# Performance work log

Measured on AMD Instinct MI355X. Metric: run time of the kernel, lower is better.

Reference implementation:

```python
import jax, jax.numpy as jnp
import numpy as np

D_MODEL = 1024
N_HEADS = 16
D_K = D_MODEL // N_HEADS


def setup_inputs() -> dict:
    key = jax.random.key(0)
    ks = jax.random.split(key, 12)
    B, S = 2, 2048
    scale = 1.0 / np.sqrt(D_MODEL)
    inp = {
        "q": jax.random.normal(ks[0], (B, S, D_MODEL), jnp.float32),
        "k": jax.random.normal(ks[1], (B, S, D_MODEL), jnp.float32),
        "v": jax.random.normal(ks[2], (B, S, D_MODEL), jnp.float32),
        "k_pe": jax.random.normal(ks[3], (N_HEADS, D_K, S), jnp.float32),
        "Wq": jax.random.normal(ks[4], (D_MODEL, D_MODEL), jnp.float32) * scale,
        "bq": jnp.zeros((D_MODEL,), jnp.float32),
        "Wk": jax.random.normal(ks[5], (D_MODEL, D_MODEL), jnp.float32) * scale,
        "bk": jnp.zeros((D_MODEL,), jnp.float32),
        "Wv": jax.random.normal(ks[6], (D_MODEL, D_MODEL), jnp.float32) * scale,
        "bv": jnp.zeros((D_MODEL,), jnp.float32),
        "Wo": jax.random.normal(ks[7], (D_MODEL, D_MODEL), jnp.float32) * scale,
        "bo": jnp.zeros((D_MODEL,), jnp.float32),
    }
    return inp


def reference(q, k, v, k_pe, Wq, bq, Wk, bk, Wv, bv, Wo, bo):
    B, S, _ = q.shape
    # projections -> [B, H, S, d_k]
    def split_heads(x):
        return x.reshape(B, S, N_HEADS, D_K).transpose(0, 2, 1, 3)
    qh = split_heads(q @ Wq + bq)
    kh = split_heads(k @ Wk + bk)
    vh = split_heads(v @ Wv + bv)
    # content scores + relative positional scores (two matmuls, summed)
    scores = jnp.einsum("bhsd,bhtd->bhst", qh, kh)
    scores = scores + jnp.einsum("bhsd,hdt->bhst", qh, k_pe)
    scores = scores / jnp.sqrt(jnp.asarray(D_K, qh.dtype))
    attn = jax.nn.softmax(scores, axis=-1)
    out = jnp.einsum("bhst,bhtd->bhsd", attn, vh)  # [B,H,S,d_k]
    out = out.transpose(0, 2, 1, 3).reshape(B, S, D_MODEL)
    return out @ Wo + bo
```

## Files before the change

### kernel.cpp

```cpp
#include <hip/hip_runtime.h>
#include <stdint.h>
#include <math.h>

typedef __bf16 bf16;
typedef __attribute__((ext_vector_type(8))) __bf16 bf16x8;
typedef __attribute__((ext_vector_type(4))) __bf16 bf16x4;
typedef __attribute__((ext_vector_type(4))) float f32x4;

#define MFMA_BF16(a, b, c) __builtin_amdgcn_mfma_f32_16x16x32_bf16((a), (b), (c), 0, 0, 0)

#if __has_builtin(__builtin_amdgcn_exp2f)
#define EXP2F __builtin_amdgcn_exp2f
#else
#define EXP2F exp2f
#endif

#define QSCALE 0.18033688011112042f

__device__ __forceinline__ void gl_lds16(const bf16* g, bf16* l) {
  __builtin_amdgcn_global_load_lds(
      (__attribute__((address_space(1))) unsigned int*)(uintptr_t)(g),
      (__attribute__((address_space(3))) unsigned int*)(l),
      16, 0, 0);
}

__global__ __launch_bounds__(256) void prep(
    const float* __restrict__ q, const float* __restrict__ k,
    const float* __restrict__ v, bf16* __restrict__ qb,
    bf16* __restrict__ kb, bf16* __restrict__ vb,
    const float* __restrict__ W0, const float* __restrict__ W1,
    const float* __restrict__ W2, const float* __restrict__ W3,
    bf16* __restrict__ Wt,
    const float* __restrict__ kpe, bf16* __restrict__ kpeb)
{
  __shared__ float tile[64][65];
  const int tid = threadIdx.x;
  const int bid = blockIdx.x;
  if (bid < 6144) {
    const int z = bid >> 11;
    const int idx = bid & 2047;
    const float* s = (z == 0) ? q : (z == 1) ? k : v;
    bf16* d = (z == 0) ? qb : (z == 1) ? kb : vb;
    size_t i = ((size_t)idx * 256 + tid) * 8;
    float4 a = *(const float4*)(s + i);
    float4 b = *(const float4*)(s + i + 4);
    bf16x8 o;
    o[0] = (bf16)a.x; o[1] = (bf16)a.y; o[2] = (bf16)a.z; o[3] = (bf16)a.w;
    o[4] = (bf16)b.x; o[5] = (bf16)b.y; o[6] = (bf16)b.z; o[7] = (bf16)b.w;
    *(bf16x8*)(d + i) = o;
  } else if (bid < 7168) {
    const int t = bid - 6144;
    const int z = t >> 8;
    const int rem = t & 255;
    const int r0 = (rem >> 4) * 64, c0 = (rem & 15) * 64;
    const float* src = (z == 0) ? W0 : (z == 1) ? W1 : (z == 2) ? W2 : W3;
    bf16* dst = Wt + (size_t)z * (1024 * 1024);
#pragma unroll
    for (int h = 0; h < 2; ++h) {
      int qq = tid + h * 256;
      int row = qq >> 3, cc = qq & 7;
      float4 a = *(const float4*)(src + (size_t)(r0 + row) * 1024 + c0 + cc * 8);
      float4 b = *(const float4*)(src + (size_t)(r0 + row) * 1024 + c0 + cc * 8 + 4);
      tile[row][cc * 8 + 0] = a.x; tile[row][cc * 8 + 1] = a.y;
      tile[row][cc * 8 + 2] = a.z; tile[row][cc * 8 + 3] = a.w;
      tile[row][cc * 8 + 4] = b.x; tile[row][cc * 8 + 5] = b.y;
      tile[row][cc * 8 + 6] = b.z; tile[row][cc * 8 + 7] = b.w;
    }
    __syncthreads();
#pragma unroll
    for (int h = 0; h < 2; ++h) {
      int qq = tid + h * 256;
      int row = qq >> 3, cc = qq & 7;
      bf16x8 o;
#pragma unroll
      for (int e = 0; e < 8; ++e) o[e] = (bf16)tile[cc * 8 + e][row];
      *(bf16x8*)(dst + (size_t)(c0 + row) * 1024 + r0 + cc * 8) = o;
    }
  } else {
    const int idx = bid - 7168;
    size_t i = ((size_t)idx * 256 + tid) * 8;
    float4 a = *(const float4*)(kpe + i);
    float4 b = *(const float4*)(kpe + i + 4);
    bf16x8 o;
    o[0] = (bf16)a.x; o[1] = (bf16)a.y; o[2] = (bf16)a.z; o[3] = (bf16)a.w;
    o[4] = (bf16)b.x; o[5] = (bf16)b.y; o[6] = (bf16)b.z; o[7] = (bf16)b.w;
    *(bf16x8*)(kpeb + i) = o;
  }
}

template <int MODE>
__device__ __forceinline__ void gemm_body(
    const bf16* __restrict__ A, const bf16* __restrict__ Wt,
    const float* __restrict__ bias, float oscale,
    const bf16* __restrict__ kpeb, void* __restrict__ out_v,
    bf16* __restrict__ As, bf16* __restrict__ Bs)
{
  const int tid = threadIdx.x;
  const int w = tid >> 6, lane = tid & 63;
  const int lm = lane & 15, quad = lane >> 4;
  const int wr = w >> 1, wc = w & 1;
  const int lid = blockIdx.x + (blockIdx.y << 3);
  const int xcd = lid & 7, j = lid >> 3;
  const int m0 = (xcd * 4 + (j & 3)) * 128;
  const int n0 = (j >> 2) * 128;

  f32x4 zero4 = {0.f, 0.f, 0.f, 0.f};
  f32x4 acc[4][4];
#pragma unroll
  for (int i = 0; i < 4; ++i)
#pragma unroll
    for (int jj = 0; jj < 4; ++jj) acc[i][jj] = zero4;

  auto stage = [&](int buf, int kb) {
#pragma unroll
    for (int h = 0; h < 2; ++h) {
      int qq = tid + h * 256;
      int row = qq >> 2, cs = qq & 3;
      int cc = cs ^ ((row >> 1) & 3);
      gl_lds16(A + (size_t)(m0 + row) * 1024 + kb * 32 + cc * 8,
               As + buf * 4096 + qq * 8);
      gl_lds16(Wt + (size_t)(n0 + row) * 1024 + kb * 32 + cc * 8,
               Bs + buf * 4096 + qq * 8);
    }
  };

  stage(0, 0);
  stage(1, 1);

  int cur = 0;
  for (int kb = 0; kb < 32; ++kb) {
    if (kb < 30) {
      stage((kb + 2) % 3, kb + 2);
      asm volatile("s_waitcnt vmcnt(8)" ::: "memory");
    } else if (kb == 30) {
      asm volatile("s_waitcnt vmcnt(4)" ::: "memory");
    } else {
      asm volatile("s_waitcnt vmcnt(0)" ::: "memory");
    }
    __builtin_amdgcn_s_barrier();
    asm volatile("" ::: "memory");

    const bf16* Ab = As + cur * 4096;
    const bf16* Bb = Bs + cur * 4096;
    bf16x8 af[4], bfv[4];
#pragma unroll
    for (int i = 0; i < 4; ++i) {
      int row = wr * 64 + i * 16 + lm;
      af[i] = *(const bf16x8*)(Ab + row * 32 + ((quad ^ ((row >> 1) & 3)) * 8));
    }
#pragma unroll
    for (int jj = 0; jj < 4; ++jj) {
      int row = wc * 64 + jj * 16 + lm;
      bfv[jj] = *(const bf16x8*)(Bb + row * 32 + ((quad ^ ((row >> 1) & 3)) * 8));
    }
#pragma unroll
    for (int i = 0; i < 4; ++i)
#pragma unroll
      for (int jj = 0; jj < 4; ++jj)
        acc[i][jj] = MFMA_BF16(af[i], bfv[jj], acc[i][jj]);

    __builtin_amdgcn_s_barrier();
    asm volatile("" ::: "memory");
    cur = (cur + 1) == 3 ? 0 : cur + 1;
  }

  const int ncol = n0 + wc * 64;
  float bv4[4];
#pragma unroll
  for (int jj = 0; jj < 4; ++jj) bv4[jj] = bias[ncol + jj * 16 + lm];
#pragma unroll
  for (int i = 0; i < 4; ++i) {
    const int mbase = m0 + wr * 64 + i * 16 + quad * 4;
    const int b = mbase >> 11, s = mbase & 2047;
#pragma unroll
    for (int jj = 0; jj < 4; ++jj) {
      const int ng = ncol + jj * 16 + lm;
      const int hh = ng >> 6, d = ng & 63;
      if (MODE == 2) {
        bf16x4 o;
#pragma unroll
        for (int r = 0; r < 4; ++r) o[r] = (bf16)(acc[i][jj][r] + bv4[jj]);
        *(bf16x4*)((bf16*)out_v + ((size_t)(b * 16 + hh) * 64 + d) * 2048 + s) = o;
      } else if (MODE == 1) {
        bf16x4 p4 = *(const bf16x4*)(kpeb + ((size_t)(hh * 64 + d)) * 2048 + s);
#pragma unroll
        for (int r = 0; r < 4; ++r) {
          float val = acc[i][jj][r] + bv4[jj] + (float)p4[r];
          ((bf16*)out_v)[(((size_t)(b * 16 + hh)) * 2048 + (s + r)) * 64 + d] =
              (bf16)val;
        }
      } else if (MODE == 0) {
#pragma unroll
        for (int r = 0; r < 4; ++r) {
          float val = acc[i][jj][r] + bv4[jj];
          ((bf16*)out_v)[(((size_t)(b * 16 + hh)) * 2048 + (s + r)) * 64 + d] =
              (bf16)(val * oscale);
        }
      } else {
#pragma unroll
        for (int r = 0; r < 4; ++r) {
          float val = acc[i][jj][r] + bv4[jj];
          ((float*)out_v)[(size_t)(mbase + r) * 1024 + ng] = val;
        }
      }
    }
  }
}

__global__ __launch_bounds__(256) void qkv_gemm(
    const bf16* __restrict__ qb, const bf16* __restrict__ kb, const bf16* __restrict__ vb,
    const bf16* __restrict__ Wt, const float* __restrict__ biq,
    const float* __restrict__ bik, const float* __restrict__ biv,
    const bf16* __restrict__ kpeb,
    bf16* __restrict__ Qs, bf16* __restrict__ Ks, bf16* __restrict__ Vts)
{
  __shared__ __align__(16) bf16 As[3 * 128 * 32];
  __shared__ __align__(16) bf16 Bs[3 * 128 * 32];
  const int z = blockIdx.z;
  if (z == 0) {
    gemm_body<0>(qb, Wt, biq, QSCALE, nullptr, Qs, As, Bs);
  } else if (z == 1) {
    gemm_body<1>(kb, Wt + (size_t)1 * 1024 * 1024, bik, 1.f, kpeb, Ks, As, Bs);
  } else {
    gemm_body<2>(vb, Wt + (size_t)2 * 1024 * 1024, biv, 1.f, nullptr, Vts, As, Bs);
  }
}

__global__ __launch_bounds__(256) void out_gemm(
    const bf16* __restrict__ A, const bf16* __restrict__ Wt,
    const float* __restrict__ bias, float* __restrict__ out)
{
  __shared__ __align__(16) bf16 As[3 * 128 * 32];
  __shared__ __align__(16) bf16 Bs[3 * 128 * 32];
  gemm_body<3>(A, Wt, bias, 1.f, nullptr, out, As, Bs);
}

__global__ __launch_bounds__(512) void flash_attn(
    const bf16* __restrict__ Q, const bf16* __restrict__ K,
    const bf16* __restrict__ Vt, bf16* __restrict__ O)
{
  __shared__ __align__(16) bf16 QtPs[128 * 72];
  __shared__ __align__(16) bf16 Kt[2][64 * 64];
  __shared__ __align__(16) bf16 Vs[2][64 * 64];
  bf16* Ps = QtPs;

  const int tid = threadIdx.x;
  const int w = tid >> 6, lane = tid & 63;
  const int lm = lane & 15, quad = lane >> 4;
  const int id = blockIdx.x;
  const int xcd = id & 7, j = id >> 3;
  const int bh = xcd * 4 + (j & 3);
  const int s0 = (j >> 2) * 128;
  const size_t qkbase = (size_t)bh * (2048 * 64);
  const size_t vbase = (size_t)bh * (64 * 2048);

#pragma unroll
  for (int h = 0; h < 2; ++h) {
    int qq = tid + h * 512;
    int row = qq >> 3, cs = qq & 7;
    int cc = cs ^ (row & 7);
    gl_lds16(Q + qkbase + (size_t)(s0 + row) * 64 + cc * 8, QtPs + qq * 8);
  }
  {
    int row = tid >> 3, cs = tid & 7;
    int cc = cs ^ (row & 7);
    gl_lds16(K + qkbase + (size_t)row * 64 + cc * 8, Kt[0] + tid * 8);
    gl_lds16(Vt + vbase + (size_t)row * 2048 + cc * 8, Vs[0] + tid * 8);
  }
  __syncthreads();

  bf16x8 qa0, qa1;
  {
    int row = w * 16 + lm;
    qa0 = *(const bf16x8*)(QtPs + row * 64 + ((quad ^ (row & 7)) * 8));
    qa1 = *(const bf16x8*)(QtPs + row * 64 + (((quad + 4) ^ (row & 7)) * 8));
  }
  __syncthreads();

  f32x4 zero4 = {0.f, 0.f, 0.f, 0.f};
  float l_part = 0.f;
  f32x4 oacc[4];
#pragma unroll
  for (int dt = 0; dt < 4; ++dt) oacc[dt] = zero4;

  const int prow = (w * 16 + lm) * 72;

  for (int kt = 0; kt < 32; ++kt) {
    const int cur = kt & 1;
    if (kt < 31) {
      const int t1 = (kt + 1) * 64;
      int row = tid >> 3, cs = tid & 7;
      int cc = cs ^ (row & 7);
      gl_lds16(K + qkbase + (size_t)(t1 + row) * 64 + cc * 8, Kt[cur ^ 1] + tid * 8);
      gl_lds16(Vt + vbase + (size_t)row * 2048 + t1 + cc * 8, Vs[cur ^ 1] + tid * 8);
    }

#pragma unroll
    for (int c = 0; c < 4; ++c) {
      int row = c * 16 + lm;
      bf16x8 kb0 = *(const bf16x8*)(Kt[cur] + row * 64 + ((quad ^ (row & 7)) * 8));
      bf16x8 kb1 = *(const bf16x8*)(Kt[cur] + row * 64 + (((quad + 4) ^ (row & 7)) * 8));
      __builtin_amdgcn_s_setprio(1);
      f32x4 z = MFMA_BF16(kb0, qa0, zero4);
      f32x4 st = MFMA_BF16(kb1, qa1, z);
      __builtin_amdgcn_s_setprio(0);
      bf16x4 pk;
#pragma unroll
      for (int r = 0; r < 4; ++r) {
        float p = EXP2F(st[r]);
        l_part += p;
        pk[r] = (bf16)p;
      }
      *(bf16x4*)(Ps + prow + c * 16 + quad * 4) = pk;
    }

    bf16x8 pa0 = *(const bf16x8*)(Ps + prow + quad * 8);
    bf16x8 pa1 = *(const bf16x8*)(Ps + prow + 32 + quad * 8);
#pragma unroll
    for (int dt = 0; dt < 4; ++dt) {
      int row = dt * 16 + lm;
      bf16x8 va0 = *(const bf16x8*)(Vs[cur] + row * 64 + ((quad ^ (row & 7)) * 8));
      bf16x8 va1 = *(const bf16x8*)(Vs[cur] + row * 64 + (((quad + 4) ^ (row & 7)) * 8));
      __builtin_amdgcn_s_setprio(1);
      oacc[dt] = MFMA_BF16(va0, pa0, oacc[dt]);
      oacc[dt] = MFMA_BF16(va1, pa1, oacc[dt]);
      __builtin_amdgcn_s_setprio(0);
    }

    __syncthreads();
  }

  float l = l_part;
  l += __shfl_xor(l, 16, 64);
  l += __shfl_xor(l, 32, 64);
  float inv = 1.f / l;
#pragma unroll
  for (int dt = 0; dt < 4; ++dt)
#pragma unroll
    for (int r = 0; r < 4; ++r)
      Ps[prow + dt * 16 + quad * 4 + r] = (bf16)(oacc[dt][r] * inv);

  const int b = bh >> 4, hh = bh & 15;
  const int srow = s0 + w * 16 + lm;
  const size_t ob = ((size_t)(b * 2048 + srow)) * 1024 + hh * 64;
#pragma unroll
  for (int half = 0; half < 2; ++half) {
    bf16x8 ov = *(const bf16x8*)(Ps + prow + (half * 4 + quad) * 8);
    *(bf16x8*)(O + ob + (half * 4 + quad) * 8) = ov;
  }
}

extern "C" void kernel_launch(void* const* d_in, const int* in_sizes, int n_in,
                              void* d_out, int out_size, void* d_ws, size_t ws_size,
                              hipStream_t stream) {
  (void)in_sizes; (void)n_in; (void)out_size; (void)ws_size;
  const float* q   = (const float*)d_in[0];
  const float* k   = (const float*)d_in[1];
  const float* v   = (const float*)d_in[2];
  const float* kpe = (const float*)d_in[3];
  const float* Wq  = (const float*)d_in[4];
  const float* bq  = (const float*)d_in[5];
  const float* Wk  = (const float*)d_in[6];
  const float* bk  = (const float*)d_in[7];
  const float* Wv  = (const float*)d_in[8];
  const float* bv  = (const float*)d_in[9];
  const float* Wo  = (const float*)d_in[10];
  const float* bo  = (const float*)d_in[11];

  const size_t NT = 4u * 1024 * 1024;
  bf16* ws  = (bf16*)d_ws;
  bf16* Wt  = ws;
  bf16* qb  = Wt + NT;
  bf16* kb  = qb + NT;
  bf16* vb  = kb + NT;
  bf16* Qs  = vb + NT;
  bf16* Ks  = Qs + NT;
  bf16* Vts = Ks + NT;
  bf16* Oa  = Vts + NT;
  bf16* kpeb = Oa;

  prep<<<dim3(8192), 256, 0, stream>>>(q, k, v, qb, kb, vb, Wq, Wk, Wv, Wo, Wt,
                                       kpe, kpeb);
  qkv_gemm<<<dim3(8, 32, 3), 256, 0, stream>>>(qb, kb, vb, Wt, bq, bk, bv, kpeb,
                                               Qs, Ks, Vts);
  flash_attn<<<dim3(512), 512, 0, stream>>>(Qs, Ks, Vts, Oa);
  out_gemm<<<dim3(8, 32), 256, 0, stream>>>(Oa, Wt + 3u * 1024 * 1024, bo,
                                            (float*)d_out);
}
```

Measured before the change: 236.4 us.

## Enlarge QKV projection GEMM tiles to 256x256 with 512-thread blocks

```diff
diff --git a/kernel.cpp b/kernel.cpp
--- a/kernel.cpp
+++ b/kernel.cpp
@@ -89,7 +89,7 @@
 }
 
 template <int MODE>
-__device__ __forceinline__ void gemm_body(
+__device__ __forceinline__ void gemm_body256(
     const bf16* __restrict__ A, const bf16* __restrict__ Wt,
     const float* __restrict__ bias, float oscale,
     const bf16* __restrict__ kpeb, void* __restrict__ out_v,
@@ -99,28 +99,28 @@
   const int w = tid >> 6, lane = tid & 63;
   const int lm = lane & 15, quad = lane >> 4;
   const int wr = w >> 1, wc = w & 1;
-  const int lid = blockIdx.x + (blockIdx.y << 3);
-  const int xcd = lid & 7, j = lid >> 3;
-  const int m0 = (xcd * 4 + (j & 3)) * 128;
-  const int n0 = (j >> 2) * 128;
+  const int lid = blockIdx.x + (blockIdx.y << 2);
+  const int xcd = lid & 7, jj = lid >> 3;
+  const int m0 = (xcd * 2 + (jj & 1)) * 256;
+  const int n0 = (jj >> 1) * 256;
 
   f32x4 zero4 = {0.f, 0.f, 0.f, 0.f};
-  f32x4 acc[4][4];
+  f32x4 acc[4][8];
 #pragma unroll
   for (int i = 0; i < 4; ++i)
 #pragma unroll
-    for (int jj = 0; jj < 4; ++jj) acc[i][jj] = zero4;
+    for (int j = 0; j < 8; ++j) acc[i][j] = zero4;
 
   auto stage = [&](int buf, int kb) {
 #pragma unroll
     for (int h = 0; h < 2; ++h) {
-      int qq = tid + h * 256;
+      int qq = tid + h * 512;
       int row = qq >> 2, cs = qq & 3;
       int cc = cs ^ ((row >> 1) & 3);
       gl_lds16(A + (size_t)(m0 + row) * 1024 + kb * 32 + cc * 8,
-               As + buf * 4096 + qq * 8);
+               As + buf * 8192 + qq * 8);
       gl_lds16(Wt + (size_t)(n0 + row) * 1024 + kb * 32 + cc * 8,
-               Bs + buf * 4096 + qq * 8);
+               Bs + buf * 8192 + qq * 8);
     }
   };
 
@@ -140,89 +140,83 @@
     __builtin_amdgcn_s_barrier();
     asm volatile("" ::: "memory");
 
-    const bf16* Ab = As + cur * 4096;
-    const bf16* Bb = Bs + cur * 4096;
-    bf16x8 af[4], bfv[4];
+    const bf16* Ab = As + cur * 8192;
+    const bf16* Bb = Bs + cur * 8192;
+    bf16x8 af[4], bfv[8];
 #pragma unroll
     for (int i = 0; i < 4; ++i) {
       int row = wr * 64 + i * 16 + lm;
       af[i] = *(const bf16x8*)(Ab + row * 32 + ((quad ^ ((row >> 1) & 3)) * 8));
     }
 #pragma unroll
-    for (int jj = 0; jj < 4; ++jj) {
-      int row = wc * 64 + jj * 16 + lm;
-      bfv[jj] = *(const bf16x8*)(Bb + row * 32 + ((quad ^ ((row >> 1) & 3)) * 8));
+    for (int j = 0; j < 8; ++j) {
+      int row = wc * 128 + j * 16 + lm;
+      bfv[j] = *(const bf16x8*)(Bb + row * 32 + ((quad ^ ((row >> 1) & 3)) * 8));
     }
 #pragma unroll
     for (int i = 0; i < 4; ++i)
 #pragma unroll
-      for (int jj = 0; jj < 4; ++jj)
-        acc[i][jj] = MFMA_BF16(af[i], bfv[jj], acc[i][jj]);
+      for (int j = 0; j < 8; ++j)
+        acc[i][j] = MFMA_BF16(af[i], bfv[j], acc[i][j]);
 
     __builtin_amdgcn_s_barrier();
     asm volatile("" ::: "memory");
     cur = (cur + 1) == 3 ? 0 : cur + 1;
   }
 
-  const int ncol = n0 + wc * 64;
-  float bv4[4];
-#pragma unroll
-  for (int jj = 0; jj < 4; ++jj) bv4[jj] = bias[ncol + jj * 16 + lm];
+  const int ncol = n0 + wc * 128;
+  float bv8[8];
+#pragma unroll
+  for (int j = 0; j < 8; ++j) bv8[j] = bias[ncol + j * 16 + lm];
 #pragma unroll
   for (int i = 0; i < 4; ++i) {
     const int mbase = m0 + wr * 64 + i * 16 + quad * 4;
     const int b = mbase >> 11, s = mbase & 2047;
 #pragma unroll
-    for (int jj = 0; jj < 4; ++jj) {
-      const int ng = ncol + jj * 16 + lm;
+    for (int j = 0; j < 8; ++j) {
+      const int ng = ncol + j * 16 + lm;
       const int hh = ng >> 6, d = ng & 63;
       if (MODE == 2) {
         bf16x4 o;
 #pragma unroll
-        for (int r = 0; r < 4; ++r) o[r] = (bf16)(acc[i][jj][r] + bv4[jj]);
+        for (int r = 0; r < 4; ++r) o[r] = (bf16)(acc[i][j][r] + bv8[j]);
         *(bf16x4*)((bf16*)out_v + ((size_t)(b * 16 + hh) * 64 + d) * 2048 + s) = o;
       } else if (MODE == 1) {
         bf16x4 p4 = *(const bf16x4*)(kpeb + ((size_t)(hh * 64 + d)) * 2048 + s);
 #pragma unroll
         for (int r = 0; r < 4; ++r) {
-          float val = acc[i][jj][r] + bv4[jj] + (float)p4[r];
+          float val = acc[i][j][r] + bv8[j] + (float)p4[r];
           ((bf16*)out_v)[(((size_t)(b * 16 + hh)) * 2048 + (s + r)) * 64 + d] =
               (bf16)val;
         }
-      } else if (MODE == 0) {
+      } else {
 #pragma unroll
         for (int r = 0; r < 4; ++r) {
-          float val = acc[i][jj][r] + bv4[jj];
+          float val = acc[i][j][r] + bv8[j];
           ((bf16*)out_v)[(((size_t)(b * 16 + hh)) * 2048 + (s + r)) * 64 + d] =
               (bf16)(val * oscale);
         }
-      } else {
-#pragma unroll
-        for (int r = 0; r < 4; ++r) {
-          float val = acc[i][jj][r] + bv4[jj];
-          ((float*)out_v)[(size_t)(mbase + r) * 1024 + ng] = val;
-        }
       }
     }
   }
 }
 
-__global__ __launch_bounds__(256) void qkv_gemm(
+__global__ __launch_bounds__(512, 2) void qkv_gemm(
     const bf16* __restrict__ qb, const bf16* __restrict__ kb, const bf16* __restrict__ vb,
     const bf16* __restrict__ Wt, const float* __restrict__ biq,
     const float* __restrict__ bik, const float* __restrict__ biv,
     const bf16* __restrict__ kpeb,
     bf16* __restrict__ Qs, bf16* __restrict__ Ks, bf16* __restrict__ Vts)
 {
-  __shared__ __align__(16) bf16 As[3 * 128 * 32];
-  __shared__ __align__(16) bf16 Bs[3 * 128 * 32];
+  __shared__ __align__(16) bf16 As[3 * 256 * 32];
+  __shared__ __align__(16) bf16 Bs[3 * 256 * 32];
   const int z = blockIdx.z;
   if (z == 0) {
-    gemm_body<0>(qb, Wt, biq, QSCALE, nullptr, Qs, As, Bs);
+    gemm_body256<0>(qb, Wt, biq, QSCALE, nullptr, Qs, As, Bs);
   } else if (z == 1) {
-    gemm_body<1>(kb, Wt + (size_t)1 * 1024 * 1024, bik, 1.f, kpeb, Ks, As, Bs);
+    gemm_body256<1>(kb, Wt + (size_t)1 * 1024 * 1024, bik, 1.f, kpeb, Ks, As, Bs);
   } else {
-    gemm_body<2>(vb, Wt + (size_t)2 * 1024 * 1024, biv, 1.f, nullptr, Vts, As, Bs);
+    gemm_body256<2>(vb, Wt + (size_t)2 * 1024 * 1024, biv, 1.f, nullptr, Vts, As, Bs);
   }
 }
 
@@ -232,7 +226,91 @@
 {
   __shared__ __align__(16) bf16 As[3 * 128 * 32];
   __shared__ __align__(16) bf16 Bs[3 * 128 * 32];
-  gemm_body<3>(A, Wt, bias, 1.f, nullptr, out, As, Bs);
+  const int tid = threadIdx.x;
+  const int w = tid >> 6, lane = tid & 63;
+  const int lm = lane & 15, quad = lane >> 4;
+  const int wr = w >> 1, wc = w & 1;
+  const int lid = blockIdx.x + (blockIdx.y << 3);
+  const int xcd = lid & 7, j = lid >> 3;
+  const int m0 = (xcd * 4 + (j & 3)) * 128;
+  const int n0 = (j >> 2) * 128;
+
+  f32x4 zero4 = {0.f, 0.f, 0.f, 0.f};
+  f32x4 acc[4][4];
+#pragma unroll
+  for (int i = 0; i < 4; ++i)
+#pragma unroll
+    for (int jj = 0; jj < 4; ++jj) acc[i][jj] = zero4;
+
+  auto stage = [&](int buf, int kb) {
+#pragma unroll
+    for (int h = 0; h < 2; ++h) {
+      int qq = tid + h * 256;
+      int row = qq >> 2, cs = qq & 3;
+      int cc = cs ^ ((row >> 1) & 3);
+      gl_lds16(A + (size_t)(m0 + row) * 1024 + kb * 32 + cc * 8,
+               As + buf * 4096 + qq * 8);
+      gl_lds16(Wt + (size_t)(n0 + row) * 1024 + kb * 32 + cc * 8,
+               Bs + buf * 4096 + qq * 8);
+    }
+  };
+
+  stage(0, 0);
+  stage(1, 1);
+
+  int cur = 0;
+  for (int kb = 0; kb < 32; ++kb) {
+    if (kb < 30) {
+      stage((kb + 2) % 3, kb + 2);
+      asm volatile("s_waitcnt vmcnt(8)" ::: "memory");
+    } else if (kb == 30) {
+      asm volatile("s_waitcnt vmcnt(4)" ::: "memory");
+    } else {
+      asm volatile("s_waitcnt vmcnt(0)" ::: "memory");
+    }
+    __builtin_amdgcn_s_barrier();
+    asm volatile("" ::: "memory");
+
+    const bf16* Ab = As + cur * 4096;
+    const bf16* Bb = Bs + cur * 4096;
+    bf16x8 af[4], bfv[4];
+#pragma unroll
+    for (int i = 0; i < 4; ++i) {
+      int row = wr * 64 + i * 16 + lm;
+      af[i] = *(const bf16x8*)(Ab + row * 32 + ((quad ^ ((row >> 1) & 3)) * 8));
+    }
+#pragma unroll
+    for (int jj = 0; jj < 4; ++jj) {
+      int row = wc * 64 + jj * 16 + lm;
+      bfv[jj] = *(const bf16x8*)(Bb + row * 32 + ((quad ^ ((row >> 1) & 3)) * 8));
+    }
+#pragma unroll
+    for (int i = 0; i < 4; ++i)
+#pragma unroll
+      for (int jj = 0; jj < 4; ++jj)
+        acc[i][jj] = MFMA_BF16(af[i], bfv[jj], acc[i][jj]);
+
+    __builtin_amdgcn_s_barrier();
+    asm volatile("" ::: "memory");
+    cur = (cur + 1) == 3 ? 0 : cur + 1;
+  }
+
+  const int ncol = n0 + wc * 64;
+  float bv4[4];
+#pragma unroll
+  for (int jj = 0; jj < 4; ++jj) bv4[jj] = bias[ncol + jj * 16 + lm];
+#pragma unroll
+  for (int i = 0; i < 4; ++i) {
+    const int mbase = m0 + wr * 64 + i * 16 + quad * 4;
+#pragma unroll
+    for (int jj = 0; jj < 4; ++jj) {
+      const int ng = ncol + jj * 16 + lm;
+#pragma unroll
+      for (int r = 0; r < 4; ++r) {
+        out[(size_t)(mbase + r) * 1024 + ng] = acc[i][jj][r] + bv4[jj];
+      }
+    }
+  }
 }
 
 __global__ __launch_bounds__(512) void flash_attn(
@@ -381,7 +459,7 @@
 
   prep<<<dim3(8192), 256, 0, stream>>>(q, k, v, qb, kb, vb, Wq, Wk, Wv, Wo, Wt,
                                        kpe, kpeb);
-  qkv_gemm<<<dim3(8, 32, 3), 256, 0, stream>>>(qb, kb, vb, Wt, bq, bk, bv, kpeb,
+  qkv_gemm<<<dim3(4, 16, 3), 512, 0, stream>>>(qb, kb, vb, Wt, bq, bk, bv, kpeb,
                                                Qs, Ks, Vts);
   flash_attn<<<dim3(512), 512, 0, stream>>>(Qs, Ks, Vts, Oa);
   out_gemm<<<dim3(8, 32), 256, 0, stream>>>(Oa, Wt + 3u * 1024 * 1024, bo,
```

Result: no change. 236.7 us (+0.1%).
